# Optimization experiments

Hardware: AMD Instinct MI355X
Metric: run time of the kernel (lower is better)

The kernel has to match this reference:

```python
import jax, jax.numpy as jnp
import numpy as np

N_NODES = 50000
N_EDGES = 800000
IN_DIM = 256
OUT_DIM = 128
ALPHA = 0.2  # leaky_relu negative slope


def setup_inputs() -> dict:
    key = jax.random.key(0)
    k1, k2, k3, k4, k5 = jax.random.split(key, 5)
    h = jax.random.normal(k1, (N_NODES, IN_DIM), dtype=jnp.float32)
    src = jax.random.randint(k2, (N_EDGES,), 0, N_NODES)
    dst = jax.random.randint(k3, (N_EDGES,), 0, N_NODES)
    W_fc = jax.random.normal(k4, (IN_DIM, OUT_DIM), dtype=jnp.float32) * (1.0 / np.sqrt(IN_DIM))
    attn_w = jax.random.normal(k5, (2 * OUT_DIM,), dtype=jnp.float32) * (1.0 / np.sqrt(2 * OUT_DIM))
    return {"h": h, "src": src, "dst": dst, "W_fc": W_fc, "attn_w": attn_w}


def reference(h, src, dst, W_fc, attn_w):
    n = h.shape[0]
    # fc projection: z = h @ W  -> [N, out]
    z = h @ W_fc
    # edge attention logit: attn_fc(cat(z_src, z_dst)) = z_src@a1 + z_dst@a2
    a1 = attn_w[:OUT_DIM]
    a2 = attn_w[OUT_DIM:]
    logit = z[src] @ a1 + z[dst] @ a2               # [E]
    e = jnp.where(logit >= 0, logit, ALPHA * logit)  # leaky_relu
    # segment softmax over incoming edges of each destination node
    m = jax.ops.segment_max(e, dst, num_segments=n)   # [N], -inf if no edges
    m = jnp.where(jnp.isfinite(m), m, 0.0)
    ex = jnp.exp(e - m[dst])                          # [E]
    denom = jax.ops.segment_sum(ex, dst, num_segments=n)  # [N]
    denom = jnp.where(denom > 0, denom, 1.0)
    alpha_e = ex / denom[dst]                         # [E]
    # weighted scatter-sum of source features
    h_out = jax.ops.segment_sum(alpha_e[:, None] * z[src], dst, num_segments=n)  # [N, out]
    # concat=True -> elu activation
    return jnp.where(h_out > 0, h_out, jnp.expm1(h_out))
```

## Files before the change

### kernel.cpp

```cpp
#include <hip/hip_runtime.h>
#include <math.h>

#define N_NODES 50000
#define N_EDGES 800000
#define IN_DIM 256
#define OUT_DIM 128
#define ALPHA 0.2f

#define BKT 196
#define EPB 4096
#define HIST_NB 196
#define GEMM_NB 391

typedef __attribute__((ext_vector_type(8))) short short8;
typedef __attribute__((ext_vector_type(4))) float f32x4;

#define OFF_ZB    0u
#define OFF_S1    12800000u
#define OFF_S2    13000000u
#define OFF_OFFS2 13200000u
#define OFF_WT    13400064u
#define OFF_HIST  13465600u
#define OFF_TMP   13619264u
#define OFF_SRCS  16819264u

static __device__ __forceinline__ unsigned short f2bf_rne(float f) {
    unsigned int u = __float_as_uint(f);
    unsigned int r = (u + 0x7FFFu + ((u >> 16) & 1u)) >> 16;
    return (unsigned short)r;
}
static __device__ __forceinline__ unsigned int pack2bf(float lo, float hi) {
    return (unsigned int)f2bf_rne(lo) | ((unsigned int)f2bf_rne(hi) << 16);
}

__global__ __launch_bounds__(256) void wt_k(const float* __restrict__ W,
                                            unsigned short* __restrict__ WT) {
    int idx = (blockIdx.x * 256 + threadIdx.x) * 8;
    int c = idx >> 8, k0 = idx & 255;
    unsigned int uu[4];
#pragma unroll
    for (int q = 0; q < 4; q++) {
        float lo = W[(size_t)(k0 + 2 * q) * OUT_DIM + c];
        float hi = W[(size_t)(k0 + 2 * q + 1) * OUT_DIM + c];
        uu[q] = pack2bf(lo, hi);
    }
    *(uint4*)(WT + idx) = make_uint4(uu[0], uu[1], uu[2], uu[3]);
}

__global__ __launch_bounds__(512) void gemm_hist(const float* __restrict__ h,
                                                 const unsigned short* __restrict__ WT,
                                                 const float* __restrict__ attn,
                                                 unsigned short* __restrict__ zb,
                                                 float* __restrict__ s1,
                                                 float* __restrict__ s2,
                                                 const int* __restrict__ dst,
                                                 int* __restrict__ histT) {
    __shared__ char smem[32768];
    const int t = threadIdx.x;

    if (blockIdx.x >= GEMM_NB) {
        int hb = blockIdx.x - GEMM_NB;
        int* hcnt = (int*)smem;
        for (int i = t; i < BKT; i += 512) hcnt[i] = 0;
        __syncthreads();
#pragma unroll
        for (int q = 0; q < 8; q++) {
            int e = hb * EPB + q * 512 + t;
            if (e < N_EDGES) atomicAdd(&hcnt[dst[e] >> 8], 1);
        }
        __syncthreads();
        for (int i = t; i < BKT; i += 512) histT[i * HIST_NB + hb] = hcnt[i];
        return;
    }

    const int lane = t & 63, w = t >> 6;
    const int row0 = blockIdx.x * 128;
    const int m16 = lane & 15, kb = lane >> 4;

    const int rA = row0 + w * 16 + m16;
    const float* hrow = h + (size_t)min(rA, N_NODES - 1) * IN_DIM + kb * 8;

    f32x4 acc[8];
#pragma unroll
    for (int ct = 0; ct < 8; ct++) acc[ct] = (f32x4){0.f, 0.f, 0.f, 0.f};

    float4 v0 = *(const float4*)(hrow);
    float4 v1 = *(const float4*)(hrow + 4);

#pragma unroll
    for (int half = 0; half < 2; half++) {
        if (half) __syncthreads();
#pragma unroll
        for (int q = 0; q < 4; q++) {
            int G = t * 4 + q;
            int cc = G >> 4, gs = G & 15;
            const uint4 v = *(const uint4*)(WT + (size_t)cc * IN_DIM + half * 128 + gs * 8);
            *(uint4*)(smem + cc * 256 + ((gs ^ (cc & 7)) * 16)) = v;
        }
        __syncthreads();
#pragma unroll
        for (int kcl = 0; kcl < 4; kcl++) {
            const float4 c0 = v0, c1 = v1;
            int nk = half * 4 + kcl + 1;
            if (nk < 8) {
                v0 = *(const float4*)(hrow + nk * 32);
                v1 = *(const float4*)(hrow + nk * 32 + 4);
            }
            short8 af;
            af[0] = (short)f2bf_rne(c0.x); af[1] = (short)f2bf_rne(c0.y);
            af[2] = (short)f2bf_rne(c0.z); af[3] = (short)f2bf_rne(c0.w);
            af[4] = (short)f2bf_rne(c1.x); af[5] = (short)f2bf_rne(c1.y);
            af[6] = (short)f2bf_rne(c1.z); af[7] = (short)f2bf_rne(c1.w);
            const char* bbase = smem + m16 * 256 + (((kcl * 4 + kb) ^ (m16 & 7)) * 16);
#pragma unroll
            for (int ct = 0; ct < 8; ct++) {
                const short8 bf = *(const short8*)(bbase + ct * 4096);
                acc[ct] = __builtin_amdgcn_mfma_f32_16x16x32_bf16(af, bf, acc[ct], 0, 0, 0);
            }
        }
    }

    float a1v[8], a2v[8];
#pragma unroll
    for (int ct = 0; ct < 8; ct++) {
        a1v[ct] = attn[ct * 16 + m16];
        a2v[ct] = attn[OUT_DIM + ct * 16 + m16];
    }
#pragma unroll
    for (int i = 0; i < 4; i++) {
        int rr = row0 + w * 16 + kb * 4 + i;
        float q1 = 0.f, q2 = 0.f;
#pragma unroll
        for (int ct = 0; ct < 8; ct++) {
            q1 += acc[ct][i] * a1v[ct];
            q2 += acc[ct][i] * a2v[ct];
        }
        q1 += __shfl_xor(q1, 1); q1 += __shfl_xor(q1, 2);
        q1 += __shfl_xor(q1, 4); q1 += __shfl_xor(q1, 8);
        q2 += __shfl_xor(q2, 1); q2 += __shfl_xor(q2, 2);
        q2 += __shfl_xor(q2, 4); q2 += __shfl_xor(q2, 8);
        if (m16 == 0 && rr < N_NODES) { s1[rr] = q1; s2[rr] = q2; }
        if (rr < N_NODES) {
#pragma unroll
            for (int ct = 0; ct < 8; ct++)
                zb[(size_t)rr * OUT_DIM + ct * 16 + m16] = f2bf_rne(acc[ct][i]);
        }
    }
}

__global__ __launch_bounds__(512) void scatter_b(const int* __restrict__ src,
                                                 const int* __restrict__ dst,
                                                 const int* __restrict__ histT,
                                                 unsigned int* __restrict__ tmp) {
    __shared__ int sS[256];
    __shared__ int bbL[BKT];
    __shared__ int bstartL[BKT];
    __shared__ int cur[BKT];
    int t = threadIdx.x, m = blockIdx.x;

    int tot = 0, bb = 0;
    if (t < BKT) {
        const int* row = histT + t * HIST_NB;
        for (int m2 = 0; m2 < BKT; m2++) {
            int v = row[m2];
            tot += v;
            bb += (m2 < m) ? v : 0;
        }
        bbL[t] = bb;
        cur[t] = 0;
    }
    int d0 = (t < BKT) ? tot : 0;
    if (t < 256) sS[t] = d0;
    __syncthreads();
    int v = d0;
    for (int ofs = 1; ofs < 256; ofs <<= 1) {
        int add = (t < 256 && t >= ofs) ? sS[t - ofs] : 0;
        __syncthreads();
        if (t < 256) { v += add; sS[t] = v; }
        __syncthreads();
    }
    if (t < BKT) bstartL[t] = v - d0;
    __syncthreads();

#pragma unroll
    for (int q = 0; q < 8; q++) {
        int e = m * EPB + q * 512 + t;
        if (e < N_EDGES) {
            int d = dst[e];
            int bkt = d >> 8;
            int r = atomicAdd(&cur[bkt], 1);
            tmp[bstartL[bkt] + bbL[bkt] + r] =
                ((unsigned int)d << 16) | (unsigned int)src[e];
        }
    }
}

__global__ __launch_bounds__(512) void bucket_sort(const unsigned int* __restrict__ tmp,
                                                   const int* __restrict__ histT,
                                                   unsigned short* __restrict__ srcs,
                                                   int* __restrict__ offs2) {
    __shared__ int sS[256];
    __shared__ int cnt[256];
    __shared__ int cur[256];
    __shared__ int msS, mcS;
    int t = threadIdx.x, b = blockIdx.x;

    int tot = 0;
    if (t < BKT) {
        const int* row = histT + t * HIST_NB;
        for (int m2 = 0; m2 < BKT; m2++) tot += row[m2];
    }
    int d0 = (t < BKT) ? tot : 0;
    if (t < 256) { sS[t] = d0; cnt[t] = 0; }
    __syncthreads();
    int v = d0;
    for (int ofs = 1; ofs < 256; ofs <<= 1) {
        int add = (t < 256 && t >= ofs) ? sS[t - ofs] : 0;
        __syncthreads();
        if (t < 256) { v += add; sS[t] = v; }
        __syncthreads();
    }
    if (t == b) { msS = v - d0; mcS = d0; }
    __syncthreads();
    const int myStart = msS, myCount = mcS;

    for (int i = t; i < myCount; i += 512)
        atomicAdd(&cnt[(tmp[myStart + i] >> 16) & 255], 1);
    __syncthreads();

    int c0 = 0;
    if (t < 256) { c0 = cnt[t]; sS[t] = c0; }
    __syncthreads();
    int cv = c0;
    for (int ofs = 1; ofs < 256; ofs <<= 1) {
        int add = (t < 256 && t >= ofs) ? sS[t - ofs] : 0;
        __syncthreads();
        if (t < 256) { cv += add; sS[t] = cv; }
        __syncthreads();
    }
    if (t < 256) {
        int excl = cv - c0;
        int node = b * 256 + t;
        if (node < N_NODES) offs2[node] = myStart + excl;
        cur[t] = excl;
    }
    if (b == 0 && t == 0) offs2[N_NODES] = N_EDGES;
    __syncthreads();

    for (int i = t; i < myCount; i += 512) {
        unsigned int u = tmp[myStart + i];
        int r = atomicAdd(&cur[(u >> 16) & 255], 1);
        srcs[myStart + r] = (unsigned short)(u & 0xFFFFu);
    }
}

__global__ __launch_bounds__(256) void aggregate(const unsigned short* __restrict__ zb,
                                                 const int* __restrict__ offs2,
                                                 const unsigned short* __restrict__ srcs,
                                                 const float* __restrict__ s1,
                                                 const float* __restrict__ s2,
                                                 float* __restrict__ out) {
    int wid = (blockIdx.x * blockDim.x + threadIdx.x) >> 6;
    int lane = threadIdx.x & 63;
    if (wid >= N_NODES) return;
    float2* outp = (float2*)(out + (size_t)wid * OUT_DIM) + lane;

    int base = offs2[wid];
    int len = offs2[wid + 1] - base;
    if (len == 0) {
        *outp = make_float2(0.f, 0.f);
        return;
    }
    const float s2v = s2[wid];
    const unsigned int voff = lane * 2;

    float sum = 0.f;
    float ax = 0.f, ay = 0.f;

    for (int c0 = 0; c0 < len; c0 += 64) {
        int i = c0 + lane;
        float ex = 0.f;
        int sj = 0;
        if (i < len) {
            sj = srcs[base + i];
            float lg = s1[sj] + s2v;
            lg = (lg >= 0.f) ? lg : ALPHA * lg;
            ex = __expf(lg);
        }
        sum += ex;
        int cnt = min(64, len - c0);
        int j = 0;
        for (; j + 4 <= cnt; j += 4) {
#pragma unroll
            for (int q = 0; q < 4; q++) {
                int s = __builtin_amdgcn_readlane(sj, j + q);
                float wj = __int_as_float(__builtin_amdgcn_readlane(__float_as_int(ex), j + q));
                unsigned int u = *(const unsigned int*)(zb + (size_t)(unsigned)s * OUT_DIM + voff);
                ax += wj * __uint_as_float(u << 16);
                ay += wj * __uint_as_float(u & 0xFFFF0000u);
            }
        }
        for (; j < cnt; j++) {
            int s = __builtin_amdgcn_readlane(sj, j);
            float wj = __int_as_float(__builtin_amdgcn_readlane(__float_as_int(ex), j));
            unsigned int u = *(const unsigned int*)(zb + (size_t)(unsigned)s * OUT_DIM + voff);
            ax += wj * __uint_as_float(u << 16);
            ay += wj * __uint_as_float(u & 0xFFFF0000u);
        }
    }
#pragma unroll
    for (int m = 32; m >= 1; m >>= 1) sum += __shfl_xor(sum, m);
    float inv = (sum > 0.f) ? 1.f / sum : 1.f;

    float a0 = ax * inv, a1 = ay * inv;
    float2 o;
    o.x = (a0 > 0.f) ? a0 : expm1f(a0);
    o.y = (a1 > 0.f) ? a1 : expm1f(a1);
    *outp = o;
}

extern "C" void kernel_launch(void* const* d_in, const int* in_sizes, int n_in,
                              void* d_out, int out_size, void* d_ws, size_t ws_size,
                              hipStream_t stream) {
    const float* h      = (const float*)d_in[0];
    const int*   src    = (const int*)d_in[1];
    const int*   dst    = (const int*)d_in[2];
    const float* W_fc   = (const float*)d_in[3];
    const float* attn_w = (const float*)d_in[4];
    float* out = (float*)d_out;

    char* ws = (char*)d_ws;
    unsigned short* zb = (unsigned short*)(ws + OFF_ZB);
    float* s1       = (float*)(ws + OFF_S1);
    float* s2       = (float*)(ws + OFF_S2);
    int*   offs2    = (int*)(ws + OFF_OFFS2);
    unsigned short* WT = (unsigned short*)(ws + OFF_WT);
    int*   histT    = (int*)(ws + OFF_HIST);
    unsigned int* tmp = (unsigned int*)(ws + OFF_TMP);
    unsigned short* srcs = (unsigned short*)(ws + OFF_SRCS);

    wt_k<<<16, 256, 0, stream>>>(W_fc, WT);
    gemm_hist<<<GEMM_NB + HIST_NB, 512, 0, stream>>>(h, WT, attn_w, zb, s1, s2, dst, histT);
    scatter_b<<<HIST_NB, 512, 0, stream>>>(src, dst, histT, tmp);
    bucket_sort<<<BKT, 512, 0, stream>>>(tmp, histT, srcs, offs2);
    aggregate<<<(N_NODES * 64) / 256, 256, 0, stream>>>(zb, offs2, srcs, s1, s2, out);
}
```

Baseline: 86.12 us.

## Merge histogram with weight transpose and scatter with GEMM, cutting launches

The edge histogram moves into the same kernel as the weight transpose, and the bucket scatter now runs as extra blocks of the GEMM kernel, so one kernel launch goes away and scatter overlaps with the GEMM. The scatter's block 0 writes the bucket starts and counts to global memory, so bucket_sort no longer rescans the histogram and runs its own prefix sum. The cost is that the scatter blocks compete with the GEMM blocks for compute units.

```diff
diff --git a/kernel.cpp b/kernel.cpp
--- a/kernel.cpp
+++ b/kernel.cpp
@@ -10,19 +10,22 @@
 #define BKT 196
 #define EPB 4096
 #define HIST_NB 196
+#define WT_NB   8
 #define GEMM_NB 391
 
 typedef __attribute__((ext_vector_type(8))) short short8;
 typedef __attribute__((ext_vector_type(4))) float f32x4;
 
-#define OFF_ZB    0u
-#define OFF_S1    12800000u
-#define OFF_S2    13000000u
-#define OFF_OFFS2 13200000u
-#define OFF_WT    13400064u
-#define OFF_HIST  13465600u
-#define OFF_TMP   13619264u
-#define OFF_SRCS  16819264u
+#define OFF_ZB     0u
+#define OFF_S1     12800000u
+#define OFF_S2     13000000u
+#define OFF_OFFS2  13200000u
+#define OFF_WT     13400064u
+#define OFF_HIST   13465600u
+#define OFF_BSTART 13619264u
+#define OFF_BCNT   13620048u
+#define OFF_TMP    13620832u
+#define OFF_SRCS   16820832u
 
 static __device__ __forceinline__ unsigned short f2bf_rne(float f) {
     unsigned int u = __float_as_uint(f);
@@ -33,43 +36,96 @@
     return (unsigned int)f2bf_rne(lo) | ((unsigned int)f2bf_rne(hi) << 16);
 }
 
-__global__ __launch_bounds__(256) void wt_k(const float* __restrict__ W,
-                                            unsigned short* __restrict__ WT) {
-    int idx = (blockIdx.x * 256 + threadIdx.x) * 8;
-    int c = idx >> 8, k0 = idx & 255;
-    unsigned int uu[4];
-#pragma unroll
-    for (int q = 0; q < 4; q++) {
-        float lo = W[(size_t)(k0 + 2 * q) * OUT_DIM + c];
-        float hi = W[(size_t)(k0 + 2 * q + 1) * OUT_DIM + c];
-        uu[q] = pack2bf(lo, hi);
-    }
-    *(uint4*)(WT + idx) = make_uint4(uu[0], uu[1], uu[2], uu[3]);
-}
-
-__global__ __launch_bounds__(512) void gemm_hist(const float* __restrict__ h,
-                                                 const unsigned short* __restrict__ WT,
-                                                 const float* __restrict__ attn,
-                                                 unsigned short* __restrict__ zb,
-                                                 float* __restrict__ s1,
-                                                 float* __restrict__ s2,
-                                                 const int* __restrict__ dst,
-                                                 int* __restrict__ histT) {
+__global__ __launch_bounds__(512) void hist_wt(const int* __restrict__ dst,
+                                               const float* __restrict__ W,
+                                               int* __restrict__ histT,
+                                               unsigned short* __restrict__ WT) {
+    __shared__ int hcnt[BKT];
+    int b = blockIdx.x, t = threadIdx.x;
+    if (b < HIST_NB) {
+        for (int i = t; i < BKT; i += 512) hcnt[i] = 0;
+        __syncthreads();
+#pragma unroll
+        for (int q = 0; q < 8; q++) {
+            int e = b * EPB + q * 512 + t;
+            if (e < N_EDGES) atomicAdd(&hcnt[dst[e] >> 8], 1);
+        }
+        __syncthreads();
+        for (int i = t; i < BKT; i += 512) histT[i * HIST_NB + b] = hcnt[i];
+    } else {
+        int idx = ((b - HIST_NB) * 512 + t) * 8;
+        int c = idx >> 8, k0 = idx & 255;
+        unsigned int uu[4];
+#pragma unroll
+        for (int q = 0; q < 4; q++) {
+            float lo = W[(size_t)(k0 + 2 * q) * OUT_DIM + c];
+            float hi = W[(size_t)(k0 + 2 * q + 1) * OUT_DIM + c];
+            uu[q] = pack2bf(lo, hi);
+        }
+        *(uint4*)(WT + idx) = make_uint4(uu[0], uu[1], uu[2], uu[3]);
+    }
+}
+
+__global__ __launch_bounds__(512) void gemm_scatter(const float* __restrict__ h,
+                                                    const unsigned short* __restrict__ WT,
+                                                    const float* __restrict__ attn,
+                                                    unsigned short* __restrict__ zb,
+                                                    float* __restrict__ s1,
+                                                    float* __restrict__ s2,
+                                                    const int* __restrict__ src,
+                                                    const int* __restrict__ dst,
+                                                    const int* __restrict__ histT,
+                                                    unsigned int* __restrict__ tmp,
+                                                    int* __restrict__ bstart,
+                                                    int* __restrict__ bcnt) {
     __shared__ char smem[32768];
     const int t = threadIdx.x;
 
     if (blockIdx.x >= GEMM_NB) {
-        int hb = blockIdx.x - GEMM_NB;
-        int* hcnt = (int*)smem;
-        for (int i = t; i < BKT; i += 512) hcnt[i] = 0;
-        __syncthreads();
+        int m = blockIdx.x - GEMM_NB;
+        int* sS      = (int*)smem;
+        int* bbL     = sS + 256;
+        int* bstartL = bbL + BKT;
+        int* cur     = bstartL + BKT;
+
+        int tot = 0, bb = 0;
+        if (t < BKT) {
+            const int* row = histT + t * HIST_NB;
+            for (int m2 = 0; m2 < BKT; m2++) {
+                int v = row[m2];
+                tot += v;
+                bb += (m2 < m) ? v : 0;
+            }
+            bbL[t] = bb;
+            cur[t] = 0;
+        }
+        int d0 = (t < BKT) ? tot : 0;
+        if (t < 256) sS[t] = d0;
+        __syncthreads();
+        int v = d0;
+        for (int ofs = 1; ofs < 256; ofs <<= 1) {
+            int add = (t < 256 && t >= ofs) ? sS[t - ofs] : 0;
+            __syncthreads();
+            if (t < 256) { v += add; sS[t] = v; }
+            __syncthreads();
+        }
+        if (t < BKT) {
+            bstartL[t] = v - d0;
+            if (m == 0) { bstart[t] = v - d0; bcnt[t] = tot; }
+        }
+        __syncthreads();
+
 #pragma unroll
         for (int q = 0; q < 8; q++) {
-            int e = hb * EPB + q * 512 + t;
-            if (e < N_EDGES) atomicAdd(&hcnt[dst[e] >> 8], 1);
-        }
-        __syncthreads();
-        for (int i = t; i < BKT; i += 512) histT[i * HIST_NB + hb] = hcnt[i];
+            int e = m * EPB + q * 512 + t;
+            if (e < N_EDGES) {
+                int d = dst[e];
+                int bkt = d >> 8;
+                int r = atomicAdd(&cur[bkt], 1);
+                tmp[bstartL[bkt] + bbL[bkt] + r] =
+                    ((unsigned int)d << 16) | (unsigned int)src[e];
+            }
+        }
         return;
     }
 
@@ -148,81 +204,20 @@
     }
 }
 
-__global__ __launch_bounds__(512) void scatter_b(const int* __restrict__ src,
-                                                 const int* __restrict__ dst,
-                                                 const int* __restrict__ histT,
-                                                 unsigned int* __restrict__ tmp) {
-    __shared__ int sS[256];
-    __shared__ int bbL[BKT];
-    __shared__ int bstartL[BKT];
-    __shared__ int cur[BKT];
-    int t = threadIdx.x, m = blockIdx.x;
-
-    int tot = 0, bb = 0;
-    if (t < BKT) {
-        const int* row = histT + t * HIST_NB;
-        for (int m2 = 0; m2 < BKT; m2++) {
-            int v = row[m2];
-            tot += v;
-            bb += (m2 < m) ? v : 0;
-        }
-        bbL[t] = bb;
-        cur[t] = 0;
-    }
-    int d0 = (t < BKT) ? tot : 0;
-    if (t < 256) sS[t] = d0;
-    __syncthreads();
-    int v = d0;
-    for (int ofs = 1; ofs < 256; ofs <<= 1) {
-        int add = (t < 256 && t >= ofs) ? sS[t - ofs] : 0;
-        __syncthreads();
-        if (t < 256) { v += add; sS[t] = v; }
-        __syncthreads();
-    }
-    if (t < BKT) bstartL[t] = v - d0;
-    __syncthreads();
-
-#pragma unroll
-    for (int q = 0; q < 8; q++) {
-        int e = m * EPB + q * 512 + t;
-        if (e < N_EDGES) {
-            int d = dst[e];
-            int bkt = d >> 8;
-            int r = atomicAdd(&cur[bkt], 1);
-            tmp[bstartL[bkt] + bbL[bkt] + r] =
-                ((unsigned int)d << 16) | (unsigned int)src[e];
-        }
-    }
-}
-
 __global__ __launch_bounds__(512) void bucket_sort(const unsigned int* __restrict__ tmp,
-                                                   const int* __restrict__ histT,
+                                                   const int* __restrict__ bstart,
+                                                   const int* __restrict__ bcnt,
                                                    unsigned short* __restrict__ srcs,
                                                    int* __restrict__ offs2) {
     __shared__ int sS[256];
     __shared__ int cnt[256];
     __shared__ int cur[256];
-    __shared__ int msS, mcS;
     int t = threadIdx.x, b = blockIdx.x;
 
-    int tot = 0;
-    if (t < BKT) {
-        const int* row = histT + t * HIST_NB;
-        for (int m2 = 0; m2 < BKT; m2++) tot += row[m2];
-    }
-    int d0 = (t < BKT) ? tot : 0;
-    if (t < 256) { sS[t] = d0; cnt[t] = 0; }
+    const int myStart = bstart[b];
+    const int myCount = bcnt[b];
+    if (t < 256) cnt[t] = 0;
     __syncthreads();
-    int v = d0;
-    for (int ofs = 1; ofs < 256; ofs <<= 1) {
-        int add = (t < 256 && t >= ofs) ? sS[t - ofs] : 0;
-        __syncthreads();
-        if (t < 256) { v += add; sS[t] = v; }
-        __syncthreads();
-    }
-    if (t == b) { msS = v - d0; mcS = d0; }
-    __syncthreads();
-    const int myStart = msS, myCount = mcS;
 
     for (int i = t; i < myCount; i += 512)
         atomicAdd(&cnt[(tmp[myStart + i] >> 16) & 255], 1);
@@ -336,12 +331,14 @@
     int*   offs2    = (int*)(ws + OFF_OFFS2);
     unsigned short* WT = (unsigned short*)(ws + OFF_WT);
     int*   histT    = (int*)(ws + OFF_HIST);
+    int*   bstart   = (int*)(ws + OFF_BSTART);
+    int*   bcnt     = (int*)(ws + OFF_BCNT);
     unsigned int* tmp = (unsigned int*)(ws + OFF_TMP);
     unsigned short* srcs = (unsigned short*)(ws + OFF_SRCS);
 
-    wt_k<<<16, 256, 0, stream>>>(W_fc, WT);
-    gemm_hist<<<GEMM_NB + HIST_NB, 512, 0, stream>>>(h, WT, attn_w, zb, s1, s2, dst, histT);
-    scatter_b<<<HIST_NB, 512, 0, stream>>>(src, dst, histT, tmp);
-    bucket_sort<<<BKT, 512, 0, stream>>>(tmp, histT, srcs, offs2);
+    hist_wt<<<HIST_NB + WT_NB, 512, 0, stream>>>(dst, W_fc, histT, WT);
+    gemm_scatter<<<GEMM_NB + HIST_NB, 512, 0, stream>>>(h, WT, attn_w, zb, s1, s2,
+                                                        src, dst, histT, tmp, bstart, bcnt);
+    bucket_sort<<<BKT, 512, 0, stream>>>(tmp, bstart, bcnt, srcs, offs2);
     aggregate<<<(N_NODES * 64) / 256, 256, 0, stream>>>(zb, offs2, srcs, s1, s2, out);
 }
```

Result: faster. 77.20 us (-10.4%).
